# Performance work log

Hardware: AMD Instinct MI355X
Metric: run time of the kernel (lower is better)

## Reference

```python
import jax, jax.numpy as jnp
import numpy as np

B, L, D, H = 1, 512, 64, 64
EPS = 1e-5


def _ln(x, w, b):
    mu = jnp.mean(x, axis=-1, keepdims=True)
    var = jnp.var(x, axis=-1, keepdims=True)
    return (x - mu) * jax.lax.rsqrt(var + EPS) * w + b


def setup_inputs() -> dict:
    key = jax.random.key(0)
    ks = jax.random.split(key, 16)
    s = 0.02
    return {
        "x": jax.random.normal(ks[0], (B, L, L, D), dtype=jnp.float32),
        "sequence_mask": jax.random.randint(ks[1], (B, L), 0, 2, dtype=jnp.int32),
        "norm_w": jnp.ones((D,), jnp.float32),
        "norm_b": jnp.zeros((D,), jnp.float32),
        "left_w": jax.random.normal(ks[2], (D, H), jnp.float32) * s,
        "left_b": jnp.zeros((H,), jnp.float32),
        "right_w": jax.random.normal(ks[3], (D, H), jnp.float32) * s,
        "right_b": jnp.zeros((H,), jnp.float32),
        "lgate_w": jax.random.normal(ks[4], (D, H), jnp.float32) * s,
        "lgate_b": jnp.ones((H,), jnp.float32),
        "rgate_w": jax.random.normal(ks[5], (D, H), jnp.float32) * s,
        "rgate_b": jnp.ones((H,), jnp.float32),
        "ogate_w": jax.random.normal(ks[6], (D, D), jnp.float32) * s,
        "ogate_b": jnp.ones((D,), jnp.float32),
        "onorm_w": jnp.ones((H,), jnp.float32),
        "onorm_b": jnp.zeros((H,), jnp.float32),
        "out_w": jax.random.normal(ks[7], (H, D), jnp.float32) * s,
        "out_b": jnp.zeros((D,), jnp.float32),
    }


def reference(x, sequence_mask, norm_w, norm_b, left_w, left_b, right_w, right_b,
              lgate_w, lgate_b, rgate_w, rgate_b, ogate_w, ogate_b,
              onorm_w, onorm_b, out_w, out_b):
    xn = _ln(x, norm_w, norm_b)                              # (B,L,L,D)
    left = xn @ left_w + left_b                              # (B,L,L,H)
    right = xn @ right_w + right_b
    m = sequence_mask.astype(xn.dtype)                       # (B,L)
    mask = (m[:, :, None] * m[:, None, :])[..., None]        # (B,L,L,1)
    left = left * mask
    right = right * mask
    left = left * jax.nn.sigmoid(xn @ lgate_w + lgate_b)
    right = right * jax.nn.sigmoid(xn @ rgate_w + rgate_b)
    out_gate = jax.nn.sigmoid(xn @ ogate_w + ogate_b)        # (B,L,L,D)
    # ingoing mix: out[i,j,d] = sum_k left[k,j,d] * right[k,i,d]
    out = jnp.einsum('bkjd,bkid->bijd', left, right)         # (B,L,L,H)
    out = _ln(out, onorm_w, onorm_b)
    out = out @ out_w + out_b                                # (B,L,L,D)
    return out * out_gate
```

## Files before the change

### kernel.cpp

```cpp
#include <hip/hip_runtime.h>


typedef __attribute__((ext_vector_type(4))) float f32x4;
typedef __attribute__((ext_vector_type(8))) __bf16 bf16x8;

__device__ __forceinline__ unsigned short f2bf(float f) {
  unsigned u = __float_as_uint(f);
  u += 0x7FFFu + ((u >> 16) & 1u);
  return (unsigned short)(u >> 16);
}
__device__ __forceinline__ float bf2f(unsigned short h) {
  return __uint_as_float(((unsigned)h) << 16);
}
__device__ __forceinline__ unsigned pk2bf(float a, float b) {
  unsigned short ua = __builtin_bit_cast(unsigned short, (__bf16)a);
  unsigned short ub = __builtin_bit_cast(unsigned short, (__bf16)b);
  return (unsigned)ua | ((unsigned)ub << 16);
}
__device__ __forceinline__ float sigm(float x) { return 1.0f / (1.0f + __expf(-x)); }

__global__ __launch_bounds__(256) void k0_prep(
    const float* __restrict__ lw, const float* __restrict__ rw,
    const float* __restrict__ lgw, const float* __restrict__ rgw,
    const float* __restrict__ ogw, unsigned short* __restrict__ wt) {
  const int t = threadIdx.x;
  #pragma unroll
  for (int e = 0; e < 80; ++e) {
    int idx = e * 256 + t;
    int n = idx >> 6, k = idx & 63;
    const float* W = (n < 64) ? lw : (n < 128) ? rw : (n < 192) ? lgw
                     : (n < 256) ? rgw : ogw;
    float v = W[k * 64 + (n & 63)];
    int el = n * 64 + ((((k >> 3) ^ (n & 7)) << 3) | (k & 7));
    wt[el] = f2bf(v);
  }
}

__global__ __launch_bounds__(512) void k1_proj(
    const float* __restrict__ x, const int* __restrict__ smask,
    const float* __restrict__ norm_w, const float* __restrict__ norm_b,
    const float* __restrict__ left_b, const float* __restrict__ right_b,
    const float* __restrict__ lgate_b, const float* __restrict__ rgate_b,
    const float* __restrict__ ogate_b, const unsigned short* __restrict__ wt,
    unsigned short* __restrict__ left_t, unsigned short* __restrict__ right_t,
    unsigned short* __restrict__ ogate) {
  __shared__ __align__(16) char ldsWt[40960];
  __shared__ __align__(16) char ldsX[16384];
  __shared__ float sNW[64], sNB[64];
  __shared__ __align__(16) float sLB[64], sRB[64], sLGB[64], sRGB[64], sOGB[64];

  const int t = threadIdx.x;
  const int c = blockIdx.x & 511;
  const int r0 = (blockIdx.x >> 9) << 7;

  #pragma unroll
  for (int i = 0; i < 5; ++i) {
    int u = t + i * 512;
    *(uint4*)(ldsWt + u * 16) = *(const uint4*)((const char*)wt + u * 16);
  }
  if (t < 64) {
    sNW[t] = norm_w[t]; sNB[t] = norm_b[t];
    sLB[t] = left_b[t]; sRB[t] = right_b[t];
    sLGB[t] = lgate_b[t]; sRGB[t] = rgate_b[t]; sOGB[t] = ogate_b[t];
  }
  __syncthreads();

  {
    const int m = t >> 2, q = t & 3;
    const float* xp = x + ((size_t)(r0 + m) * 512 + c) * 64 + q * 16;
    float v[16];
    #pragma unroll
    for (int i = 0; i < 4; ++i) {
      float4 f = *(const float4*)(xp + i * 4);
      v[i*4+0] = f.x; v[i*4+1] = f.y; v[i*4+2] = f.z; v[i*4+3] = f.w;
    }
    float s = 0.f, ss = 0.f;
    #pragma unroll
    for (int i = 0; i < 16; ++i) { s += v[i]; ss += v[i] * v[i]; }
    s += __shfl_xor(s, 1); s += __shfl_xor(s, 2);
    ss += __shfl_xor(ss, 1); ss += __shfl_xor(ss, 2);
    const float mu = s * 0.015625f;
    const float rs = rsqrtf(ss * 0.015625f - mu * mu + 1e-5f);
    unsigned pk[8];
    #pragma unroll
    for (int i = 0; i < 8; ++i) {
      const int d0 = q * 16 + 2 * i;
      pk[i] = pk2bf((v[2*i]   - mu) * rs * sNW[d0]     + sNB[d0],
                    (v[2*i+1] - mu) * rs * sNW[d0 + 1] + sNB[d0 + 1]);
    }
    uint4 lo; lo.x = pk[0]; lo.y = pk[1]; lo.z = pk[2]; lo.w = pk[3];
    uint4 hi; hi.x = pk[4]; hi.y = pk[5]; hi.z = pk[6]; hi.w = pk[7];
    *(uint4*)(ldsX + m * 128 + (((q * 2)     ^ (m & 7)) << 4)) = lo;
    *(uint4*)(ldsX + m * 128 + (((q * 2 + 1) ^ (m & 7)) << 4)) = hi;
  }
  __syncthreads();

  const int w = t >> 6, l = t & 63, lr = l & 15, g = l >> 4;
  f32x4 acc[20];
  #pragma unroll
  for (int nf = 0; nf < 20; ++nf) acc[nf] = (f32x4){0.f, 0.f, 0.f, 0.f};
  const int rowA = w * 16 + lr;
  #pragma unroll
  for (int s = 0; s < 2; ++s) {
    const int soff = (((s * 4 + g) ^ (lr & 7)) << 4);
    bf16x8 a = *(const bf16x8*)(ldsX + rowA * 128 + soff);
    #pragma unroll
    for (int nf = 0; nf < 16; ++nf) {
      bf16x8 bb = *(const bf16x8*)(ldsWt + (nf * 16 + lr) * 128 + soff);
      acc[nf] = __builtin_amdgcn_mfma_f32_16x16x32_bf16(a, bb, acc[nf], 0, 0, 0);
    }
    #pragma unroll
    for (int nf = 16; nf < 20; ++nf) {
      bf16x8 bb = *(const bf16x8*)(ldsWt + (nf * 16 + lr) * 128 + soff);
      acc[nf] = __builtin_amdgcn_mfma_f32_16x16x32_bf16(bb, a, acc[nf], 0, 0, 0);
    }
  }

  const int rbase = r0 + w * 16 + g * 4;
  const float mc = (float)smask[c];
  float mk[4];
  #pragma unroll
  for (int rr = 0; rr < 4; ++rr) mk[rr] = mc * (float)smask[rbase + rr];

  const int chnk = ((rbase >> 3) ^ (c & 7));
  const size_t cb = (size_t)c * 512 + (size_t)(chnk << 3) + (size_t)(rbase & 7);
  #pragma unroll
  for (int nf = 0; nf < 4; ++nf) {
    const int hh = nf * 16 + lr;
    const float lb = sLB[hh], rb = sRB[hh];
    const float lgb = sLGB[hh], rgb = sRGB[hh];
    float lo[4], ro[4];
    #pragma unroll
    for (int rr = 0; rr < 4; ++rr) {
      lo[rr] = (acc[nf][rr]     + lb) * mk[rr] * sigm(acc[8  + nf][rr] + lgb);
      ro[rr] = (acc[4 + nf][rr] + rb) * mk[rr] * sigm(acc[12 + nf][rr] + rgb);
    }
    const size_t base = (size_t)hh * 262144 + cb;
    uint2 lv; lv.x = pk2bf(lo[0], lo[1]); lv.y = pk2bf(lo[2], lo[3]);
    uint2 rv; rv.x = pk2bf(ro[0], ro[1]); rv.y = pk2bf(ro[2], ro[3]);
    *(uint2*)(left_t + base)  = lv;
    *(uint2*)(right_t + base) = rv;
  }

  const size_t pog = ((size_t)(r0 + w * 16 + lr) * 512 + c) * 64;
  #pragma unroll
  for (int nf = 0; nf < 4; ++nf) {
    const int d0 = nf * 16 + g * 4;
    const float4 ob4 = *(const float4*)&sOGB[d0];
    const float g0 = sigm(acc[16 + nf][0] + ob4.x);
    const float g1 = sigm(acc[16 + nf][1] + ob4.y);
    const float g2 = sigm(acc[16 + nf][2] + ob4.z);
    const float g3 = sigm(acc[16 + nf][3] + ob4.w);
    uint2 gv; gv.x = pk2bf(g0, g1); gv.y = pk2bf(g2, g3);
    *(uint2*)(ogate + pog + d0) = gv;
  }
}

__global__ __launch_bounds__(256) void k2_einsum(
    const unsigned short* __restrict__ left_t,
    const unsigned short* __restrict__ right_t,
    unsigned short* __restrict__ o) {
  __shared__ __align__(16) char ldsA[16384];
  __shared__ __align__(16) char ldsB[16384];
  const int t = threadIdx.x;
  const int d = blockIdx.x >> 4;
  const int i0 = ((blockIdx.x >> 2) & 3) * 128;
  const int j0 = (blockIdx.x & 3) * 128;
  const int w = t >> 6, l = t & 63, lr = l & 15, g = l >> 4;
  const char* Rb = (const char*)right_t + (size_t)d * 524288;
  const char* Lb = (const char*)left_t  + (size_t)d * 524288;
  f32x4 acc[4][4];
  #pragma unroll
  for (int mi = 0; mi < 4; ++mi)
    #pragma unroll
    for (int nj = 0; nj < 4; ++nj) acc[mi][nj] = (f32x4){0.f, 0.f, 0.f, 0.f};
  const int wm0 = (w >> 1) * 64, wn0 = (w & 1) * 64;
  for (int kb = 0; kb < 512; kb += 64) {
    #pragma unroll
    for (int cc = 0; cc < 4; ++cc) {
      const int p16 = (w * 4 + cc) * 64 + l;
      const int m = p16 >> 3, sl = p16 & 7;
      *(uint4*)(ldsA + p16 * 16) =
          *(const uint4*)(Rb + (size_t)(i0 + m) * 1024 + kb * 2 + sl * 16);
      *(uint4*)(ldsB + p16 * 16) =
          *(const uint4*)(Lb + (size_t)(j0 + m) * 1024 + kb * 2 + sl * 16);
    }
    __syncthreads();
    #pragma unroll
    for (int s = 0; s < 2; ++s) {
      const int soff = (((s * 4 + g) ^ (lr & 7)) << 4);
      bf16x8 af[4], bfr[4];
      #pragma unroll
      for (int mi = 0; mi < 4; ++mi)
        af[mi] = *(const bf16x8*)(ldsA + (wm0 + mi * 16 + lr) * 128 + soff);
      #pragma unroll
      for (int nj = 0; nj < 4; ++nj)
        bfr[nj] = *(const bf16x8*)(ldsB + (wn0 + nj * 16 + lr) * 128 + soff);
      #pragma unroll
      for (int mi = 0; mi < 4; ++mi)
        #pragma unroll
        for (int nj = 0; nj < 4; ++nj)
          acc[mi][nj] = __builtin_amdgcn_mfma_f32_16x16x32_bf16(
              af[mi], bfr[nj], acc[mi][nj], 0, 0, 0);
    }
    __syncthreads();
  }
  #pragma unroll
  for (int mi = 0; mi < 4; ++mi)
    #pragma unroll
    for (int nj = 0; nj < 4; ++nj)
      #pragma unroll
      for (int rr = 0; rr < 4; ++rr) {
        const int i = i0 + wm0 + mi * 16 + g * 4 + rr;
        const int j = j0 + wn0 + nj * 16 + lr;
        o[(size_t)d * 262144 + (size_t)i * 512 + j] = f2bf(acc[mi][nj][rr]);
      }
}

__global__ __launch_bounds__(256) void k3_final(
    const unsigned short* __restrict__ o, const unsigned short* __restrict__ ogate,
    const float* __restrict__ onorm_w, const float* __restrict__ onorm_b,
    const float* __restrict__ out_w, const float* __restrict__ out_b,
    float* __restrict__ out) {
  __shared__ __align__(16) char ldsO[64 * 272];
  __shared__ __align__(16) float ldsW[64 * 68];
  __shared__ float sONW[64], sONB[64], sOB[64];
  const int t = threadIdx.x;
  const int i = blockIdx.x >> 2;
  const int j0 = (blockIdx.x & 3) << 7;
  const size_t p0 = (size_t)i * 512 + j0;

  #pragma unroll
  for (int e = 0; e < 4; ++e) {
    const int u = t + e * 256;
    const int d = u >> 4, sl = u & 15;
    *(uint4*)(ldsO + d * 272 + sl * 16) =
        *(const uint4*)((const char*)o + ((size_t)d * 262144 + p0) * 2 + sl * 16);
  }
  #pragma unroll
  for (int e = 0; e < 16; ++e) {
    const int idx = e * 256 + t;
    ldsW[(idx >> 6) * 68 + (idx & 63)] = out_w[idx];
  }
  if (t < 64) { sONW[t] = onorm_w[t]; sONB[t] = onorm_b[t]; sOB[t] = out_b[t]; }
  __syncthreads();

  const int p = t >> 1, h = t & 1;
  float v[32];
  #pragma unroll
  for (int dl = 0; dl < 32; ++dl)
    v[dl] = bf2f(*(const unsigned short*)(ldsO + (h * 32 + dl) * 272 + p * 2));
  float s = 0.f, ss = 0.f;
  #pragma unroll
  for (int dl = 0; dl < 32; ++dl) { s += v[dl]; ss += v[dl] * v[dl]; }
  s += __shfl_xor(s, 1); ss += __shfl_xor(ss, 1);
  const float mu = s * 0.015625f;
  const float rs = rsqrtf(ss * 0.015625f - mu * mu + 1e-5f);
  float xv[32];
  #pragma unroll
  for (int dl = 0; dl < 32; ++dl) {
    const int d = h * 32 + dl;
    xv[dl] = (v[dl] - mu) * rs * sONW[d] + sONB[d];
  }

  const int n0 = h * 32;
  float acc[32];
  #pragma unroll
  for (int n = 0; n < 32; ++n) acc[n] = 0.f;
  #pragma unroll 4
  for (int kk = 0; kk < 32; ++kk) {
    const float a = xv[kk];
    const float* wr = ldsW + (h * 32 + kk) * 68 + n0;
    #pragma unroll
    for (int c = 0; c < 8; ++c) {
      const float4 wv = *(const float4*)(wr + c * 4);
      acc[c*4+0] += a * wv.x; acc[c*4+1] += a * wv.y;
      acc[c*4+2] += a * wv.z; acc[c*4+3] += a * wv.w;
    }
  }
  #pragma unroll 4
  for (int kk = 0; kk < 32; ++kk) {
    const float a = __shfl_xor(xv[kk], 1);
    const float* wr = ldsW + ((1 - h) * 32 + kk) * 68 + n0;
    #pragma unroll
    for (int c = 0; c < 8; ++c) {
      const float4 wv = *(const float4*)(wr + c * 4);
      acc[c*4+0] += a * wv.x; acc[c*4+1] += a * wv.y;
      acc[c*4+2] += a * wv.z; acc[c*4+3] += a * wv.w;
    }
  }

  const size_t pl = p0 + p;
  const unsigned short* gp = ogate + pl * 64 + n0;
  float* op = out + pl * 64 + n0;
  #pragma unroll
  for (int c = 0; c < 4; ++c) {
    const uint4 g4 = *(const uint4*)(gp + c * 8);
    const unsigned gg[4] = {g4.x, g4.y, g4.z, g4.w};
    float r[8];
    #pragma unroll
    for (int e = 0; e < 4; ++e) {
      r[2*e]   = (acc[c*8 + 2*e]   + sOB[n0 + c*8 + 2*e])   *
                 bf2f((unsigned short)(gg[e] & 0xffffu));
      r[2*e+1] = (acc[c*8 + 2*e+1] + sOB[n0 + c*8 + 2*e+1]) *
                 bf2f((unsigned short)(gg[e] >> 16));
    }
    float4 s0; s0.x = r[0]; s0.y = r[1]; s0.z = r[2]; s0.w = r[3];
    float4 s1; s1.x = r[4]; s1.y = r[5]; s1.z = r[6]; s1.w = r[7];
    *(float4*)(op + c * 8)     = s0;
    *(float4*)(op + c * 8 + 4) = s1;
  }
}

extern "C" void kernel_launch(void* const* d_in, const int* in_sizes, int n_in,
                              void* d_out, int out_size, void* d_ws, size_t ws_size,
                              hipStream_t stream) {
  const float* x       = (const float*)d_in[0];
  const int*   sm      = (const int*)d_in[1];
  const float* norm_w  = (const float*)d_in[2];
  const float* norm_b  = (const float*)d_in[3];
  const float* left_w  = (const float*)d_in[4];
  const float* left_b  = (const float*)d_in[5];
  const float* right_w = (const float*)d_in[6];
  const float* right_b = (const float*)d_in[7];
  const float* lgate_w = (const float*)d_in[8];
  const float* lgate_b = (const float*)d_in[9];
  const float* rgate_w = (const float*)d_in[10];
  const float* rgate_b = (const float*)d_in[11];
  const float* ogate_w = (const float*)d_in[12];
  const float* ogate_b = (const float*)d_in[13];
  const float* onorm_w = (const float*)d_in[14];
  const float* onorm_b = (const float*)d_in[15];
  const float* out_w   = (const float*)d_in[16];
  const float* out_b   = (const float*)d_in[17];

  char* ws = (char*)d_ws;
  unsigned short* left_t  = (unsigned short*)(ws + 0);
  unsigned short* right_t = (unsigned short*)(ws + 33554432);
  unsigned short* ogate   = (unsigned short*)(ws + 67108864);
  unsigned short* obuf    = (unsigned short*)(ws + 100663296);
  unsigned short* wt      = (unsigned short*)(ws + 134217728);

  if (ws_size < (size_t)134217728 + 40960) return;

  k0_prep<<<dim3(1), dim3(256), 0, stream>>>(left_w, right_w, lgate_w, rgate_w,
                                             ogate_w, wt);
  k1_proj<<<dim3(2048), dim3(512), 0, stream>>>(x, sm, norm_w, norm_b, left_b,
                                                right_b, lgate_b, rgate_b,
                                                ogate_b, wt, left_t, right_t,
                                                ogate);
  k2_einsum<<<dim3(1024), dim3(256), 0, stream>>>(left_t, right_t, obuf);
  k3_final<<<dim3(2048), dim3(256), 0, stream>>>(obuf, ogate, onorm_w, onorm_b,
                                                 out_w, out_b, (float*)d_out);
}
```

Before: 145.8 us.

## Split projection GEMM into three phases to cut accumulator registers and LDS

The fused projection kernel used to compute all 20 output fragments (left, right, both gates, output gate) at once. It now runs three sequential phases: left+left-gate, then right+right-gate, then output gate, each with at most 8 accumulators. The weight table is reordered so each phase's weights are contiguous, and the weights are streamed into two reused 16KB LDS buffers while earlier phases compute. The mask is staged in LDS. This is meant to lower VGPR and LDS pressure and raise occupancy on the memory-bound pass, at the cost of extra block barriers and serialized phases.

New measurement: 149.1 us. +2.3%, slower.

```diff
diff --git a/kernel.cpp b/kernel.cpp
--- a/kernel.cpp
+++ b/kernel.cpp
@@ -28,7 +28,7 @@
   for (int e = 0; e < 80; ++e) {
     int idx = e * 256 + t;
     int n = idx >> 6, k = idx & 63;
-    const float* W = (n < 64) ? lw : (n < 128) ? rw : (n < 192) ? lgw
+    const float* W = (n < 64) ? lw : (n < 128) ? lgw : (n < 192) ? rw
                      : (n < 256) ? rgw : ogw;
     float v = W[k * 64 + (n & 63)];
     int el = n * 64 + ((((k >> 3) ^ (n & 7)) << 3) | (k & 7));
@@ -44,26 +44,28 @@
     const float* __restrict__ ogate_b, const unsigned short* __restrict__ wt,
     unsigned short* __restrict__ left_t, unsigned short* __restrict__ right_t,
     unsigned short* __restrict__ ogate) {
-  __shared__ __align__(16) char ldsWt[40960];
+  __shared__ __align__(16) char ldsWa[16384];
+  __shared__ __align__(16) char ldsWb[16384];
   __shared__ __align__(16) char ldsX[16384];
   __shared__ float sNW[64], sNB[64];
   __shared__ __align__(16) float sLB[64], sRB[64], sLGB[64], sRGB[64], sOGB[64];
+  __shared__ float sMK[128];
 
   const int t = threadIdx.x;
   const int c = blockIdx.x & 511;
   const int r0 = (blockIdx.x >> 9) << 7;
 
   #pragma unroll
-  for (int i = 0; i < 5; ++i) {
+  for (int i = 0; i < 2; ++i) {
     int u = t + i * 512;
-    *(uint4*)(ldsWt + u * 16) = *(const uint4*)((const char*)wt + u * 16);
+    *(uint4*)(ldsWa + u * 16) = *(const uint4*)((const char*)wt + u * 16);
   }
   if (t < 64) {
     sNW[t] = norm_w[t]; sNB[t] = norm_b[t];
     sLB[t] = left_b[t]; sRB[t] = right_b[t];
     sLGB[t] = lgate_b[t]; sRGB[t] = rgate_b[t]; sOGB[t] = ogate_b[t];
   }
-  __syncthreads();
+  if (t >= 64 && t < 192) sMK[t - 64] = (float)smask[r0 + (t - 64)];
 
   {
     const int m = t >> 2, q = t & 3;
@@ -85,8 +87,8 @@
     #pragma unroll
     for (int i = 0; i < 8; ++i) {
       const int d0 = q * 16 + 2 * i;
-      pk[i] = pk2bf((v[2*i]   - mu) * rs * sNW[d0]     + sNB[d0],
-                    (v[2*i+1] - mu) * rs * sNW[d0 + 1] + sNB[d0 + 1]);
+      pk[i] = pk2bf((v[2*i]   - mu) * rs * norm_w[d0]     + norm_b[d0],
+                    (v[2*i+1] - mu) * rs * norm_w[d0 + 1] + norm_b[d0 + 1]);
     }
     uint4 lo; lo.x = pk[0]; lo.y = pk[1]; lo.z = pk[2]; lo.w = pk[3];
     uint4 hi; hi.x = pk[4]; hi.y = pk[5]; hi.z = pk[6]; hi.w = pk[7];
@@ -96,61 +98,96 @@
   __syncthreads();
 
   const int w = t >> 6, l = t & 63, lr = l & 15, g = l >> 4;
-  f32x4 acc[20];
-  #pragma unroll
-  for (int nf = 0; nf < 20; ++nf) acc[nf] = (f32x4){0.f, 0.f, 0.f, 0.f};
   const int rowA = w * 16 + lr;
+  const int rbase = r0 + w * 16 + g * 4;
+  const int chnk = ((rbase >> 3) ^ (c & 7));
+  const size_t cb = (size_t)c * 512 + (size_t)(chnk << 3) + (size_t)(rbase & 7);
+  const float mc = (float)smask[c];
+  float mk[4];
+  #pragma unroll
+  for (int rr = 0; rr < 4; ++rr) mk[rr] = mc * sMK[w * 16 + g * 4 + rr];
+
+  f32x4 acc[8];
+
+  #pragma unroll
+  for (int nf = 0; nf < 8; ++nf) acc[nf] = (f32x4){0.f, 0.f, 0.f, 0.f};
   #pragma unroll
   for (int s = 0; s < 2; ++s) {
     const int soff = (((s * 4 + g) ^ (lr & 7)) << 4);
     bf16x8 a = *(const bf16x8*)(ldsX + rowA * 128 + soff);
     #pragma unroll
-    for (int nf = 0; nf < 16; ++nf) {
-      bf16x8 bb = *(const bf16x8*)(ldsWt + (nf * 16 + lr) * 128 + soff);
+    for (int nf = 0; nf < 8; ++nf) {
+      bf16x8 bb = *(const bf16x8*)(ldsWa + (nf * 16 + lr) * 128 + soff);
       acc[nf] = __builtin_amdgcn_mfma_f32_16x16x32_bf16(a, bb, acc[nf], 0, 0, 0);
     }
-    #pragma unroll
-    for (int nf = 16; nf < 20; ++nf) {
-      bf16x8 bb = *(const bf16x8*)(ldsWt + (nf * 16 + lr) * 128 + soff);
-      acc[nf] = __builtin_amdgcn_mfma_f32_16x16x32_bf16(bb, a, acc[nf], 0, 0, 0);
-    }
-  }
-
-  const int rbase = r0 + w * 16 + g * 4;
-  const float mc = (float)smask[c];
-  float mk[4];
-  #pragma unroll
-  for (int rr = 0; rr < 4; ++rr) mk[rr] = mc * (float)smask[rbase + rr];
-
-  const int chnk = ((rbase >> 3) ^ (c & 7));
-  const size_t cb = (size_t)c * 512 + (size_t)(chnk << 3) + (size_t)(rbase & 7);
+  }
+  #pragma unroll
+  for (int i = 0; i < 2; ++i) {
+    int u = t + i * 512;
+    *(uint4*)(ldsWb + u * 16) = *(const uint4*)((const char*)wt + 16384 + u * 16);
+  }
   #pragma unroll
   for (int nf = 0; nf < 4; ++nf) {
     const int hh = nf * 16 + lr;
-    const float lb = sLB[hh], rb = sRB[hh];
-    const float lgb = sLGB[hh], rgb = sRGB[hh];
-    float lo[4], ro[4];
-    #pragma unroll
-    for (int rr = 0; rr < 4; ++rr) {
-      lo[rr] = (acc[nf][rr]     + lb) * mk[rr] * sigm(acc[8  + nf][rr] + lgb);
-      ro[rr] = (acc[4 + nf][rr] + rb) * mk[rr] * sigm(acc[12 + nf][rr] + rgb);
-    }
-    const size_t base = (size_t)hh * 262144 + cb;
+    const float lb = sLB[hh], lgb = sLGB[hh];
+    float lo[4];
+    #pragma unroll
+    for (int rr = 0; rr < 4; ++rr)
+      lo[rr] = (acc[nf][rr] + lb) * mk[rr] * sigm(acc[4 + nf][rr] + lgb);
     uint2 lv; lv.x = pk2bf(lo[0], lo[1]); lv.y = pk2bf(lo[2], lo[3]);
+    *(uint2*)(left_t + (size_t)hh * 262144 + cb) = lv;
+  }
+  __syncthreads();
+
+  #pragma unroll
+  for (int nf = 0; nf < 8; ++nf) acc[nf] = (f32x4){0.f, 0.f, 0.f, 0.f};
+  #pragma unroll
+  for (int s = 0; s < 2; ++s) {
+    const int soff = (((s * 4 + g) ^ (lr & 7)) << 4);
+    bf16x8 a = *(const bf16x8*)(ldsX + rowA * 128 + soff);
+    #pragma unroll
+    for (int nf = 0; nf < 8; ++nf) {
+      bf16x8 bb = *(const bf16x8*)(ldsWb + (nf * 16 + lr) * 128 + soff);
+      acc[nf] = __builtin_amdgcn_mfma_f32_16x16x32_bf16(a, bb, acc[nf], 0, 0, 0);
+    }
+  }
+  {
+    *(uint4*)(ldsWa + t * 16) = *(const uint4*)((const char*)wt + 32768 + t * 16);
+  }
+  #pragma unroll
+  for (int nf = 0; nf < 4; ++nf) {
+    const int hh = nf * 16 + lr;
+    const float rb = sRB[hh], rgb = sRGB[hh];
+    float ro[4];
+    #pragma unroll
+    for (int rr = 0; rr < 4; ++rr)
+      ro[rr] = (acc[nf][rr] + rb) * mk[rr] * sigm(acc[4 + nf][rr] + rgb);
     uint2 rv; rv.x = pk2bf(ro[0], ro[1]); rv.y = pk2bf(ro[2], ro[3]);
-    *(uint2*)(left_t + base)  = lv;
-    *(uint2*)(right_t + base) = rv;
-  }
-
+    *(uint2*)(right_t + (size_t)hh * 262144 + cb) = rv;
+  }
+  __syncthreads();
+
+  #pragma unroll
+  for (int nf = 0; nf < 4; ++nf) acc[nf] = (f32x4){0.f, 0.f, 0.f, 0.f};
+  #pragma unroll
+  for (int s = 0; s < 2; ++s) {
+    const int soff = (((s * 4 + g) ^ (lr & 7)) << 4);
+    bf16x8 a = *(const bf16x8*)(ldsX + rowA * 128 + soff);
+    #pragma unroll
+    for (int nf = 0; nf < 4; ++nf) {
+      bf16x8 bb = *(const bf16x8*)(ldsWa + (nf * 16 + lr) * 128 + soff);
+      acc[nf] = __builtin_amdgcn_mfma_f32_16x16x32_bf16(bb, a, acc[nf], 0, 0, 0);
+    }
+  }
   const size_t pog = ((size_t)(r0 + w * 16 + lr) * 512 + c) * 64;
   #pragma unroll
   for (int nf = 0; nf < 4; ++nf) {
     const int d0 = nf * 16 + g * 4;
     const float4 ob4 = *(const float4*)&sOGB[d0];
-    const float g0 = sigm(acc[16 + nf][0] + ob4.x);
-    const float g1 = sigm(acc[16 + nf][1] + ob4.y);
-    const float g2 = sigm(acc[16 + nf][2] + ob4.z);
-    const float g3 = sigm(acc[16 + nf][3] + ob4.w);
+    const float g0 = sigm(acc[nf][0] + ob4.x);
+    const float g1 = sigm(acc[nf][1] + ob4.y);
+    const float g2 = sigm(acc[nf][2] + ob4.z);
+    const float g3 = sigm(acc[nf][3] + ob4.w);
     uint2 gv; gv.x = pk2bf(g0, g1); gv.y = pk2bf(g2, g3);
     *(uint2*)(ogate + pog + d0) = gv;
   }
```

## Stage projection outputs through LDS for coalesced 16-byte global stores

Applied to the files above, without the earlier changes.

The projection kernel now writes its masked and gated left/right values and the output gate into shared memory, then copies them to global memory as contiguous 16-byte chunks. Before, each lane issued scattered 8-byte stores with large strides across the head dimension. The output-gate buffer is stored transposed (column-major over the pair index) so each block's writes are contiguous, and the final kernel's gate read index is changed to match. It reuses the weight and x LDS buffers, which costs extra barriers, and the final kernel's gate reads may now be less coalesced.

New measurement: 146.4 us. No clear change (+0.4%).

```diff
diff --git a/kernel.cpp b/kernel.cpp
--- a/kernel.cpp
+++ b/kernel.cpp
@@ -48,6 +48,7 @@
   __shared__ __align__(16) char ldsX[16384];
   __shared__ float sNW[64], sNB[64];
   __shared__ __align__(16) float sLB[64], sRB[64], sLGB[64], sRGB[64], sOGB[64];
+  __shared__ float sMK[128];
 
   const int t = threadIdx.x;
   const int c = blockIdx.x & 511;
@@ -63,6 +64,7 @@
     sLB[t] = left_b[t]; sRB[t] = right_b[t];
     sLGB[t] = lgate_b[t]; sRGB[t] = rgate_b[t]; sOGB[t] = ogate_b[t];
   }
+  if (t >= 64 && t < 192) sMK[t - 64] = (float)smask[r0 + (t - 64)];
   __syncthreads();
 
   {
@@ -115,44 +117,64 @@
       acc[nf] = __builtin_amdgcn_mfma_f32_16x16x32_bf16(bb, a, acc[nf], 0, 0, 0);
     }
   }
-
-  const int rbase = r0 + w * 16 + g * 4;
-  const float mc = (float)smask[c];
-  float mk[4];
-  #pragma unroll
-  for (int rr = 0; rr < 4; ++rr) mk[rr] = mc * (float)smask[rbase + rr];
-
-  const int chnk = ((rbase >> 3) ^ (c & 7));
-  const size_t cb = (size_t)c * 512 + (size_t)(chnk << 3) + (size_t)(rbase & 7);
-  #pragma unroll
-  for (int nf = 0; nf < 4; ++nf) {
-    const int hh = nf * 16 + lr;
-    const float lb = sLB[hh], rb = sRB[hh];
-    const float lgb = sLGB[hh], rgb = sRGB[hh];
-    float lo[4], ro[4];
-    #pragma unroll
-    for (int rr = 0; rr < 4; ++rr) {
-      lo[rr] = (acc[nf][rr]     + lb) * mk[rr] * sigm(acc[8  + nf][rr] + lgb);
-      ro[rr] = (acc[4 + nf][rr] + rb) * mk[rr] * sigm(acc[12 + nf][rr] + rgb);
-    }
-    const size_t base = (size_t)hh * 262144 + cb;
-    uint2 lv; lv.x = pk2bf(lo[0], lo[1]); lv.y = pk2bf(lo[2], lo[3]);
-    uint2 rv; rv.x = pk2bf(ro[0], ro[1]); rv.y = pk2bf(ro[2], ro[3]);
-    *(uint2*)(left_t + base)  = lv;
-    *(uint2*)(right_t + base) = rv;
-  }
-
-  const size_t pog = ((size_t)(r0 + w * 16 + lr) * 512 + c) * 64;
-  #pragma unroll
-  for (int nf = 0; nf < 4; ++nf) {
-    const int d0 = nf * 16 + g * 4;
-    const float4 ob4 = *(const float4*)&sOGB[d0];
-    const float g0 = sigm(acc[16 + nf][0] + ob4.x);
-    const float g1 = sigm(acc[16 + nf][1] + ob4.y);
-    const float g2 = sigm(acc[16 + nf][2] + ob4.z);
-    const float g3 = sigm(acc[16 + nf][3] + ob4.w);
-    uint2 gv; gv.x = pk2bf(g0, g1); gv.y = pk2bf(g2, g3);
-    *(uint2*)(ogate + pog + d0) = gv;
+  __syncthreads();
+
+  char* bL = ldsWt;
+  char* bR = ldsWt + 17408;
+  {
+    const float mc = (float)smask[c];
+    float mk[4];
+    #pragma unroll
+    for (int rr = 0; rr < 4; ++rr) mk[rr] = mc * sMK[w * 16 + g * 4 + rr];
+    const int rb2 = (w * 16 + g * 4) * 2;
+    #pragma unroll
+    for (int nf = 0; nf < 4; ++nf) {
+      const int hh = nf * 16 + lr;
+      const float lb = sLB[hh], rb = sRB[hh];
+      const float lgb = sLGB[hh], rgb = sRGB[hh];
+      float lo[4], ro[4];
+      #pragma unroll
+      for (int rr = 0; rr < 4; ++rr) {
+        lo[rr] = (acc[nf][rr]     + lb) * mk[rr] * sigm(acc[8  + nf][rr] + lgb);
+        ro[rr] = (acc[4 + nf][rr] + rb) * mk[rr] * sigm(acc[12 + nf][rr] + rgb);
+      }
+      uint2 lv; lv.x = pk2bf(lo[0], lo[1]); lv.y = pk2bf(lo[2], lo[3]);
+      uint2 rv; rv.x = pk2bf(ro[0], ro[1]); rv.y = pk2bf(ro[2], ro[3]);
+      *(uint2*)(bL + hh * 272 + rb2) = lv;
+      *(uint2*)(bR + hh * 272 + rb2) = rv;
+    }
+    const int rloc = w * 16 + lr;
+    #pragma unroll
+    for (int nf = 0; nf < 4; ++nf) {
+      const int d0 = nf * 16 + g * 4;
+      const float4 ob4 = *(const float4*)&sOGB[d0];
+      const float g0 = sigm(acc[16 + nf][0] + ob4.x);
+      const float g1 = sigm(acc[16 + nf][1] + ob4.y);
+      const float g2 = sigm(acc[16 + nf][2] + ob4.z);
+      const float g3 = sigm(acc[16 + nf][3] + ob4.w);
+      uint2 gv; gv.x = pk2bf(g0, g1); gv.y = pk2bf(g2, g3);
+      const int slot = (d0 >> 3) ^ (rloc & 7);
+      *(uint2*)(ldsX + rloc * 128 + slot * 16 + (d0 & 4) * 2) = gv;
+    }
+  }
+  __syncthreads();
+
+  const int cx = c & 7;
+  #pragma unroll
+  for (int it = 0; it < 2; ++it) {
+    const int idx = it * 512 + t;
+    const int hh = idx >> 4, rel = idx & 15;
+    const size_t goff = (size_t)hh * 524288 + (size_t)c * 1024 +
+                        (size_t)(((r0 >> 3) + (rel & 8) + ((rel & 7) ^ cx)) << 4);
+    *(uint4*)((char*)left_t  + goff) = *(const uint4*)(bL + hh * 272 + rel * 16);
+    *(uint4*)((char*)right_t + goff) = *(const uint4*)(bR + hh * 272 + rel * 16);
+  }
+  #pragma unroll
+  for (int it = 0; it < 2; ++it) {
+    const int idx = it * 512 + t;
+    const int rl = idx >> 3, ch = idx & 7;
+    *(uint4*)((char*)ogate + ((size_t)c * 512 + r0 + rl) * 128 + ch * 16) =
+        *(const uint4*)(ldsX + rl * 128 + ((ch ^ (rl & 7)) << 4));
   }
 }
 
@@ -290,9 +312,8 @@
     }
   }
 
-  const size_t pl = p0 + p;
-  const unsigned short* gp = ogate + pl * 64 + n0;
-  float* op = out + pl * 64 + n0;
+  const unsigned short* gp = ogate + ((size_t)(j0 + p) * 512 + i) * 64 + n0;
+  float* op = out + (p0 + p) * 64 + n0;
   #pragma unroll
   for (int c = 0; c < 4; ++c) {
     const uint4 g4 = *(const uint4*)(gp + c * 8);
```
